# Performance work log

Measured on AMD Instinct MI355X. Metric: run time of the kernel, lower is better.

## Reference

```python
import jax, jax.numpy as jnp
import numpy as np


def setup_inputs() -> dict:
    key = jax.random.key(0)
    x = jax.random.normal(key, (8, 2048, 3), dtype=jnp.float32)
    return {"x": x, "k": 16}


def reference(x, k):
    b, n, d = x.shape
    xf = x.reshape(b * n, d)                      # flatten across batch, as in the torch module
    sq = jnp.sum(xf * xf, axis=1, keepdims=True)  # [BN, 1]
    pair = 2.0 * (xf @ xf.T) - sq - sq.T          # [BN, BN] = -dist^2
    # torch topk(largest=False) on pair == largest of (-pair) == largest squared distance
    neg_vals, idx = jax.lax.top_k(-pair, k + 1)   # [BN, k+1]
    dists = -neg_vals
    dists = dists[:, 1:].reshape(b, n, k)
    idx = idx[:, 1:].reshape(b, n, k)
    return dists, idx
```

## Files before the change

### kernel.cpp

```cpp
#include <hip/hip_runtime.h>
#include <stdint.h>

#define BN       16384
#define NTILES   256
#define NB       64
#define KOUT     16
#define MARGIN   0.01f
#define PPT      16

typedef float v2f __attribute__((ext_vector_type(2)));
union F4 { float4 f4; v2f p[2]; float f[4]; };

#define WS_TAB    0
#define WS_IDX    (WS_TAB + BN * 16)
#define WS_BND    (WS_IDX + BN * 4)

__device__ __forceinline__ unsigned key_u(unsigned u) {
    return u ^ ((unsigned)((int)u >> 31) | 0x80000000u);
}
__device__ __forceinline__ unsigned wshr1(unsigned v, unsigned oldv) {
    return (unsigned)__builtin_amdgcn_update_dpp((int)oldv, (int)v, 0x138 ,
                                                 0xF, 0xF, false);
}
#define RL16(T) __uint_as_float((unsigned)__builtin_amdgcn_readlane(__float_as_int(T), 16))

__device__ __forceinline__ float sq_of(float gx, float gy, float gz) {
    return __fadd_rn(__fadd_rn(__fmul_rn(gx, gx), __fmul_rn(gy, gy)), __fmul_rn(gz, gz));
}
__device__ __forceinline__ int bucket_of(float sq) {
    const float rho = __fsqrt_rn(sq);
    int b = (int)(64.0f * (1.0f - rho * 0.2f));
    return (b < 0) ? 0 : ((b > 63) ? 63 : b);
}

#define DRAIN(m, p, jvec, T, J)                                                     \
    while (m) {                                                                     \
        const int b_ = (int)__builtin_ctzll(m);                                     \
        m &= m - 1;                                                                 \
        const float pc_ = __uint_as_float(                                          \
            (unsigned)__builtin_amdgcn_readlane(__float_as_int(p), b_));            \
        const unsigned jc_ = (unsigned)__builtin_amdgcn_readlane((int)(jvec), b_);  \
        const float Tup_ =                                                          \
            __uint_as_float(wshr1(__float_as_uint(T), 0xFF800000u ));       \
        const unsigned Jup_ = wshr1((J), 0u);                                       \
        const bool lt_ = (pc_ < Tup_) || ((pc_ == Tup_) && (jc_ < Jup_));           \
        const float Tn_ = lt_ ? Tup_ : pc_;                                         \
        const unsigned Jn_ = lt_ ? Jup_ : jc_;                                      \
        const bool sel_ = (pc_ < (T)) || ((pc_ == (T)) && (jc_ < (J)));             \
        (T) = sel_ ? Tn_ : (T);                                                     \
        (J) = sel_ ? Jn_ : (J);                                                     \
    }

#define EVALC(c, d2)                                                                \
    asm("v_pk_mul_f32 %0, %1, %2 op_sel:[0,0] op_sel_hi:[0,1]"                      \
        : "=v"(d2) : "v"((c).p[0]), "v"(c0A));                                      \
    asm("v_pk_fma_f32 %0, %1, %2, %0 op_sel:[1,0,0] op_sel_hi:[1,1,1]"              \
        : "+v"(d2) : "v"((c).p[0]), "v"(c1A));                                      \
    asm("v_pk_fma_f32 %0, %1, %2, %0 op_sel:[0,0,0] op_sel_hi:[0,1,1]"              \
        : "+v"(d2) : "v"((c).p[1]), "v"(c2A));                                      \
    asm("v_pk_add_f32 %0, %0, %1" : "+v"(d2) : "v"(nsq01));                         \
    asm("v_pk_add_f32 %0, %0, %1 op_sel:[0,1] op_sel_hi:[1,1]"                      \
        : "+v"(d2) : "v"((c).p[1]));

#define TILE_AT(t)                                                                  \
    F4 c; c.f4 = tab[(t) * 64 + lane];                                              \
    const unsigned jvec = idxarr[(t) * 64 + lane];                                  \
    v2f d2; EVALC(c, d2)

#define PROCESS_LOADED()                                                            \
    do {                                                                            \
        uint64_t m0 = __ballot(d2[0] <= fF0);                                       \
        uint64_t m1 = __ballot(d2[1] <= fF1);                                       \
        if (m0 | m1) {                                                              \
            const float p0 = d2[0], p1 = d2[1];                                     \
            DRAIN(m0, p0, jvec, T0, J0)                                             \
            DRAIN(m1, p1, jvec, T1, J1)                                             \
            fF0 = RL16(T0); thr0 = __fsub_rn(-fF0, MARGIN);                         \
            fF1 = RL16(T1); thr1 = __fsub_rn(-fF1, MARGIN);                         \
        }                                                                           \
    } while (0)

__device__ __forceinline__ void presort64(float p, unsigned j, int lane, double* sw,
                                          float& T, unsigned& J) {
    const double dm = (double)key_u(__float_as_uint(p)) * 16384.0 + (double)j;
    sw[lane] = dm;
    unsigned rank = 0;
    const char* sb = (const char*)sw;
    unsigned off = (unsigned)lane * 8u;
#pragma unroll 7
    for (int s = 1; s < 64; ++s) {
        off = (off + 8u) & 511u;
        const double dn = *(const double*)(sb + off);
        rank += (dn < dm) ? 1u : 0u;
    }
    sw[rank] = __longlong_as_double(
        (long long)(((unsigned long long)j << 32) | __float_as_uint(p)));
    const unsigned long long v = (unsigned long long)__double_as_longlong(sw[lane]);
    T = __uint_as_float((unsigned)(v & 0xFFFFFFFFull));
    J = (unsigned)(v >> 32);
}

__global__ __launch_bounds__(1024) void k_prep(const float* __restrict__ x,
                                               float4* __restrict__ tab,
                                               unsigned* __restrict__ idxarr,
                                               float2* __restrict__ bnd) {
    __shared__ unsigned hist[NB];
    __shared__ unsigned curs[NB];
    __shared__ unsigned tmaxs[NTILES];
    const int tid = threadIdx.x;
    if (tid < NB) hist[tid] = 0u;
    if (tid < NTILES) tmaxs[tid] = 0u;
    __syncthreads();

    float px[PPT], py[PPT], pz[PPT], psq[PPT];
    int pb[PPT];
#pragma unroll
    for (int k = 0; k < PPT; ++k) {
        const int i = tid + k * 1024;
        const float gx = x[3 * i], gy = x[3 * i + 1], gz = x[3 * i + 2];
        const float sq = sq_of(gx, gy, gz);
        px[k] = gx; py[k] = gy; pz[k] = gz; psq[k] = sq;
        pb[k] = bucket_of(sq);
        atomicAdd(&hist[pb[k]], 1u);
    }
    __syncthreads();
    if (tid == 0) {
        unsigned s = 0;
        for (int b = 0; b < NB; ++b) { curs[b] = s; s += hist[b]; }
    }
    __syncthreads();
#pragma unroll
    for (int k = 0; k < PPT; ++k) {
        const int i = tid + k * 1024;
        const unsigned pos = atomicAdd(&curs[pb[k]], 1u);
        tab[pos] = make_float4(px[k], py[k], pz[k], -psq[k]);
        idxarr[pos] = (unsigned)i;
        atomicMax(&tmaxs[pos >> 6], __float_as_uint(psq[k]));
    }
    __syncthreads();
    for (int s = 1; s < NTILES; s <<= 1) {
        unsigned v = 0;
        if (tid < NTILES) {
            v = tmaxs[tid];
            if (tid + s < NTILES) { const unsigned w = tmaxs[tid + s]; v = (w > v) ? w : v; }
        }
        __syncthreads();
        if (tid < NTILES) tmaxs[tid] = v;
        __syncthreads();
    }
    if (tid < NTILES) {
        const float B = __uint_as_float(tmaxs[tid]);
        const float sqB_up = __uint_as_float(__float_as_uint(__fsqrt_rn(B)) + 2u);
        bnd[tid] = make_float2(B, sqB_up);
    }
}

__global__ __launch_bounds__(256) void knn_far_kernel(
    const float* __restrict__ x, const float4* __restrict__ tab,
    const unsigned* __restrict__ idxarr, const float2* __restrict__ bnd,
    float* __restrict__ out_d, float* __restrict__ out_i) {
    __shared__ double swall[4 * 64];
    const int tid  = threadIdx.x;
    const int lane = tid & 63;
    const int wid  = tid >> 6;
    double* sw = swall + wid * 64;
    const int q0 = (blockIdx.x * 4 + wid) * 2;
    const int q1 = q0 + 1;

    const float a0 = x[3 * q0], a1 = x[3 * q0 + 1], a2 = x[3 * q0 + 2];
    const float b0 = x[3 * q1], b1 = x[3 * q1 + 1], b2 = x[3 * q1 + 2];
    const float sq0 = sq_of(a0, a1, a2), sq1 = sq_of(b0, b1, b2);
    const v2f nsq01 = {-sq0, -sq1};
    const v2f c0A = {2.0f * a0, 2.0f * b0};
    const v2f c1A = {2.0f * a1, 2.0f * b1};
    const v2f c2A = {2.0f * a2, 2.0f * b2};
    const float twor0 = 2.0f * __uint_as_float(__float_as_uint(__fsqrt_rn(sq0)) + 2u);
    const float twor1 = 2.0f * __uint_as_float(__float_as_uint(__fsqrt_rn(sq1)) + 2u);

    float T0, T1; unsigned J0, J1;
    float fF0, fF1, thr0, thr1;

    {
        TILE_AT(0)
        presort64(d2[0], jvec, lane, sw, T0, J0);
        presort64(d2[1], jvec, lane, sw, T1, J1);
        fF0 = RL16(T0); thr0 = __fsub_rn(-fF0, MARGIN);
        fF1 = RL16(T1); thr1 = __fsub_rn(-fF1, MARGIN);
    }
#pragma unroll
    for (int t = 1; t < 4; ++t) {
        TILE_AT(t)
        PROCESS_LOADED();
    }
    for (int t = 4; t < NTILES; ++t) {
        const float2 bd = bnd[t];
        const float u0 = __builtin_fmaf(twor0, bd.y, __fadd_rn(sq0, bd.x));
        const float u1 = __builtin_fmaf(twor1, bd.y, __fadd_rn(sq1, bd.x));
        if (u0 < thr0 && u1 < thr1) break;
        TILE_AT(t)
        PROCESS_LOADED();
    }

    if (lane >= 1 && lane <= KOUT) {
        const int r = lane - 1;
        out_d[q0 * KOUT + r] = T0;
        out_i[q0 * KOUT + r] = (float)J0;
        out_d[q1 * KOUT + r] = T1;
        out_i[q1 * KOUT + r] = (float)J1;
    }
}

extern "C" void kernel_launch(void* const* d_in, const int* in_sizes, int n_in,
                              void* d_out, int out_size, void* d_ws, size_t ws_size,
                              hipStream_t stream) {
    const float* x = (const float*)d_in[0];
    char* ws = (char*)d_ws;
    float4*   tab    = (float4*)(ws + WS_TAB);
    unsigned* idxarr = (unsigned*)(ws + WS_IDX);
    float2*   bnd    = (float2*)(ws + WS_BND);
    float* out_d = (float*)d_out;
    float* out_i = out_d + (size_t)BN * KOUT;

    hipLaunchKernelGGL(k_prep, dim3(1), dim3(1024), 0, stream, x, tab, idxarr, bnd);
    hipLaunchKernelGGL(knn_far_kernel, dim3(BN / 8), dim3(256), 0, stream,
                       x, tab, idxarr, bnd, out_d, out_i);
}
```

Before: 91.32 us.

## Split single-block bucket sort prep into parallel histogram, scan, and scatter kernels

Replaces the one-block, 1024-thread preparation kernel with three kernels: a 64-block per-block histogram with per-bucket max norms, a single-block prefix scan that also derives per-tile bounds from suffix bucket maxima, and a 64-block scatter. The goal is to remove the serial single-CU bottleneck of bucketing all 16384 points. In exchange it adds two kernel launches and global round-trips. The tile bounds become looser, because each is a suffix max over buckets rather than an exact per-tile max, and this may weaken pruning in the main kernel.

```diff
diff --git a/kernel.cpp b/kernel.cpp
--- a/kernel.cpp
+++ b/kernel.cpp
@@ -6,7 +6,6 @@
 #define NB       64
 #define KOUT     16
 #define MARGIN   0.01f
-#define PPT      16
 
 typedef float v2f __attribute__((ext_vector_type(2)));
 union F4 { float4 f4; v2f p[2]; float f[4]; };
@@ -14,6 +13,9 @@
 #define WS_TAB    0
 #define WS_IDX    (WS_TAB + BN * 16)
 #define WS_BND    (WS_IDX + BN * 4)
+#define WS_HIST   (WS_BND + NTILES * 8)
+#define WS_HMAX   (WS_HIST + 64 * NB * 4)
+#define WS_CBASE  (WS_HMAX + 64 * NB * 4)
 
 __device__ __forceinline__ unsigned key_u(unsigned u) {
     return u ^ ((unsigned)((int)u >> 31) | 0x80000000u);
@@ -100,59 +102,84 @@
     J = (unsigned)(v >> 32);
 }
 
-__global__ __launch_bounds__(1024) void k_prep(const float* __restrict__ x,
-                                               float4* __restrict__ tab,
-                                               unsigned* __restrict__ idxarr,
-                                               float2* __restrict__ bnd) {
-    __shared__ unsigned hist[NB];
-    __shared__ unsigned curs[NB];
-    __shared__ unsigned tmaxs[NTILES];
+__global__ __launch_bounds__(256) void k_hist(const float* __restrict__ x,
+                                              unsigned* __restrict__ hist,
+                                              unsigned* __restrict__ hmax) {
+    __shared__ unsigned h[NB], m[NB];
     const int tid = threadIdx.x;
-    if (tid < NB) hist[tid] = 0u;
-    if (tid < NTILES) tmaxs[tid] = 0u;
-    __syncthreads();
-
-    float px[PPT], py[PPT], pz[PPT], psq[PPT];
-    int pb[PPT];
-#pragma unroll
-    for (int k = 0; k < PPT; ++k) {
-        const int i = tid + k * 1024;
-        const float gx = x[3 * i], gy = x[3 * i + 1], gz = x[3 * i + 2];
-        const float sq = sq_of(gx, gy, gz);
-        px[k] = gx; py[k] = gy; pz[k] = gz; psq[k] = sq;
-        pb[k] = bucket_of(sq);
-        atomicAdd(&hist[pb[k]], 1u);
+    if (tid < NB) { h[tid] = 0u; m[tid] = 0u; }
+    __syncthreads();
+    const int i = blockIdx.x * 256 + tid;
+    const float sq = sq_of(x[3 * i], x[3 * i + 1], x[3 * i + 2]);
+    const int b = bucket_of(sq);
+    atomicAdd(&h[b], 1u);
+    atomicMax(&m[b], __float_as_uint(sq));
+    __syncthreads();
+    if (tid < NB) {
+        hist[blockIdx.x * NB + tid] = h[tid];
+        hmax[blockIdx.x * NB + tid] = m[tid];
+    }
+}
+
+__global__ __launch_bounds__(256) void k_mid(const unsigned* __restrict__ hist,
+                                             const unsigned* __restrict__ hmax,
+                                             unsigned* __restrict__ cbase,
+                                             float2* __restrict__ bnd) {
+    __shared__ unsigned tot[NB], basev[NB + 1], sfx[NB];
+    const int tid = threadIdx.x;
+    if (tid < NB) {
+        unsigned s = 0, mx = 0;
+        for (int g = 0; g < 64; ++g) {
+            s += hist[g * NB + tid];
+            const unsigned w = hmax[g * NB + tid];
+            mx = (w > mx) ? w : mx;
+        }
+        tot[tid] = s;
+        sfx[tid] = mx;
     }
     __syncthreads();
     if (tid == 0) {
         unsigned s = 0;
-        for (int b = 0; b < NB; ++b) { curs[b] = s; s += hist[b]; }
-    }
-    __syncthreads();
-#pragma unroll
-    for (int k = 0; k < PPT; ++k) {
-        const int i = tid + k * 1024;
-        const unsigned pos = atomicAdd(&curs[pb[k]], 1u);
-        tab[pos] = make_float4(px[k], py[k], pz[k], -psq[k]);
-        idxarr[pos] = (unsigned)i;
-        atomicMax(&tmaxs[pos >> 6], __float_as_uint(psq[k]));
-    }
-    __syncthreads();
-    for (int s = 1; s < NTILES; s <<= 1) {
-        unsigned v = 0;
-        if (tid < NTILES) {
-            v = tmaxs[tid];
-            if (tid + s < NTILES) { const unsigned w = tmaxs[tid + s]; v = (w > v) ? w : v; }
+        for (int b = 0; b < NB; ++b) { basev[b] = s; s += tot[b]; }
+        basev[NB] = s;
+        unsigned M = 0;
+        for (int b = NB - 1; b >= 0; --b) { const unsigned w = sfx[b]; M = (w > M) ? w : M; sfx[b] = M; }
+    }
+    __syncthreads();
+    if (tid < NB) {
+        unsigned s = basev[tid];
+        for (int g = 0; g < 64; ++g) {
+            cbase[g * NB + tid] = s;
+            s += hist[g * NB + tid];
         }
-        __syncthreads();
-        if (tid < NTILES) tmaxs[tid] = v;
-        __syncthreads();
-    }
-    if (tid < NTILES) {
-        const float B = __uint_as_float(tmaxs[tid]);
+    }
+    {
+        const unsigned pos = (unsigned)tid * 64u;
+        int b = 0;
+        for (int bb = 0; bb < NB; ++bb)
+            if (basev[bb] <= pos && pos < basev[bb + 1]) b = bb;
+        const float B = __uint_as_float(sfx[b]);
         const float sqB_up = __uint_as_float(__float_as_uint(__fsqrt_rn(B)) + 2u);
         bnd[tid] = make_float2(B, sqB_up);
     }
+}
+
+__global__ __launch_bounds__(256) void k_scatter(const float* __restrict__ x,
+                                                 const unsigned* __restrict__ cbase,
+                                                 float4* __restrict__ tab,
+                                                 unsigned* __restrict__ idxarr) {
+    __shared__ unsigned c[NB];
+    const int tid = threadIdx.x;
+    if (tid < NB) c[tid] = 0u;
+    __syncthreads();
+    const int i = blockIdx.x * 256 + tid;
+    const float gx = x[3 * i], gy = x[3 * i + 1], gz = x[3 * i + 2];
+    const float sq = sq_of(gx, gy, gz);
+    const int b = bucket_of(sq);
+    const unsigned r = atomicAdd(&c[b], 1u);
+    const unsigned pos = cbase[blockIdx.x * NB + b] + r;
+    tab[pos] = make_float4(gx, gy, gz, -sq);
+    idxarr[pos] = (unsigned)i;
 }
 
 __global__ __launch_bounds__(256) void knn_far_kernel(
@@ -218,10 +245,15 @@
     float4*   tab    = (float4*)(ws + WS_TAB);
     unsigned* idxarr = (unsigned*)(ws + WS_IDX);
     float2*   bnd    = (float2*)(ws + WS_BND);
+    unsigned* hist   = (unsigned*)(ws + WS_HIST);
+    unsigned* hmax   = (unsigned*)(ws + WS_HMAX);
+    unsigned* cbase  = (unsigned*)(ws + WS_CBASE);
     float* out_d = (float*)d_out;
     float* out_i = out_d + (size_t)BN * KOUT;
 
-    hipLaunchKernelGGL(k_prep, dim3(1), dim3(1024), 0, stream, x, tab, idxarr, bnd);
+    hipLaunchKernelGGL(k_hist,    dim3(64), dim3(256), 0, stream, x, hist, hmax);
+    hipLaunchKernelGGL(k_mid,     dim3(1),  dim3(256), 0, stream, hist, hmax, cbase, bnd);
+    hipLaunchKernelGGL(k_scatter, dim3(64), dim3(256), 0, stream, x, cbase, tab, idxarr);
     hipLaunchKernelGGL(knn_far_kernel, dim3(BN / 8), dim3(256), 0, stream,
                        x, tab, idxarr, bnd, out_d, out_i);
 }
```

Result: faster. 83.07 us, median of 2 (-9.0%).
